# Performance work log

Measured on AMD Instinct MI355X. Metric: run time of the kernel, lower is better.

## Reference

```python
import jax, jax.numpy as jnp
from jax import lax
import numpy as np

B, T, I, H, STEPS = 512, 256, 64, 512, 10


def setup_inputs() -> dict:
    key = jax.random.key(0)
    ks = jax.random.split(key, 11)
    k = 1.0 / np.sqrt(H)  # PyTorch default init bound
    u = lambda kk, shape: jax.random.uniform(kk, shape, jnp.float32, -k, k)
    return dict(
        x=jax.random.normal(ks[0], (B, T, I), jnp.float32),
        W_ih0=u(ks[1], (4 * H, I)), W_hh0=u(ks[2], (4 * H, H)),
        b_ih0=u(ks[3], (4 * H,)), b_hh0=u(ks[4], (4 * H,)),
        W_ih1=u(ks[5], (4 * H, H)), W_hh1=u(ks[6], (4 * H, H)),
        b_ih1=u(ks[7], (4 * H,)), b_hh1=u(ks[8], (4 * H,)),
        W_lin=u(ks[9], (I, H)), b_lin=u(ks[10], (I,)),
        future_steps=STEPS,
    )


def _cell(x_t, h, c, W_ih, W_hh, b):
    # PyTorch LSTM gate order: i, f, g, o
    gates = x_t @ W_ih.T + h @ W_hh.T + b
    i, f, g, o = jnp.split(gates, 4, axis=-1)
    c_new = jax.nn.sigmoid(f) * c + jax.nn.sigmoid(i) * jnp.tanh(g)
    h_new = jax.nn.sigmoid(o) * jnp.tanh(c_new)
    return h_new, c_new


def _layer_scan(xs, W_ih, W_hh, b):
    # xs: [B, T, D] -> outputs [B, T, H], final (h, c)
    Bsz, Hd = xs.shape[0], W_hh.shape[1]
    h0 = jnp.zeros((Bsz, Hd), xs.dtype)

    def step(carry, x_t):
        h, c = _cell(x_t, carry[0], carry[1], W_ih, W_hh, b)
        return (h, c), h

    (h, c), ys = lax.scan(step, (h0, h0), jnp.swapaxes(xs, 0, 1))
    return jnp.swapaxes(ys, 0, 1), (h, c)


def reference(x, W_ih0, W_hh0, b_ih0, b_hh0, W_ih1, W_hh1, b_ih1, b_hh1, W_lin, b_lin, future_steps):
    b0 = b_ih0 + b_hh0
    b1 = b_ih1 + b_hh1
    # encoder pass over the conditioning sequence
    ys0, (h0f, c0f) = _layer_scan(x, W_ih0, W_hh0, b0)
    _, (h1f, c1f) = _layer_scan(ys0, W_ih1, W_hh1, b1)
    inp = x[:, -1, :]

    def dec_step(carry, _):
        cur, h0, c0, h1, c1 = carry
        h0, c0 = _cell(cur, h0, c0, W_ih0, W_hh0, b0)
        h1, c1 = _cell(h0, h1, c1, W_ih1, W_hh1, b1)
        out = h1 @ W_lin.T + b_lin  # [B, I]
        return (out, h0, c0, h1, c1), out

    _, outs = lax.scan(dec_step, (inp, h0f, c0f, h1f, c1f), None, length=future_steps)
    return jnp.swapaxes(outs, 0, 1)  # [B, future_steps, I]
```

## Files before the change

kernel.cpp:

```cpp
#include <hip/hip_runtime.h>
#include <stdint.h>

#define BSZ 512
#define TT  256
#define IIN 64
#define HH  512
#define NSTEPS 10
#define NBLOCKS 512

typedef unsigned short ushort_t;
typedef short bf16x8 __attribute__((ext_vector_type(8)));
typedef float f32x4  __attribute__((ext_vector_type(4)));

static constexpr size_t W0TILE = 256*576;
static constexpr size_t W1TILE = 256*1024;
static constexpr size_t N0W = 8*W0TILE;
static constexpr size_t NTW = N0W + 8*W1TILE;

__device__ __forceinline__ ushort_t f2bf(float f){
  union { float f; uint32_t u; } v; v.f = f;
  uint32_t u = v.u;
  return (ushort_t)((u + 0x7fffu + ((u >> 16) & 1u)) >> 16);
}
__device__ __forceinline__ float bf2f(ushort_t h){
  union { uint32_t u; float f; } v; v.u = ((uint32_t)h) << 16;
  return v.f;
}
__device__ __forceinline__ void split2(float f, ushort_t& h, ushort_t& l){
  h = f2bf(f); l = f2bf(f - bf2f(h));
}
__device__ __forceinline__ float sigf(float x){ return 1.0f/(1.0f+__expf(-x)); }
__device__ __forceinline__ float tanhfast(float x){ return 1.0f - 2.0f/(__expf(2.0f*x)+1.0f); }

__device__ __forceinline__ unsigned long long aload64(const uint32_t* p){
  return __hip_atomic_load((const unsigned long long*)(const void*)p,
                           __ATOMIC_RELAXED, __HIP_MEMORY_SCOPE_AGENT);
}
__device__ __forceinline__ void astore32(uint32_t* p, uint32_t v){
  __hip_atomic_store(p, v, __ATOMIC_RELAXED, __HIP_MEMORY_SCOPE_AGENT);
}

__device__ __forceinline__ int get_xcd(){
  unsigned v;
  asm volatile("s_getreg_b32 %0, hwreg(HW_REG_XCC_ID)" : "=s"(v));
  return (int)(v & 7);
}

struct KP {
  const float* x;
  const ushort_t *Wh, *Wl;
  const float *b0v, *b1v;
  const float *Wlin, *blin;
  uint32_t *h0a, *h0b, *h1a, *h1b;
  float *c0m, *c1m;
  uint32_t *outp;
  float* out;
  uint32_t *bar, *rel, *assign;
};

__device__ __forceinline__ int lds_base(int c, int r){ return (c*16 + r)*64; }

__device__ __forceinline__ void stage_packed(ushort_t* lds, const uint32_t* src,
    int rowbase, int stride, int lognu, int cbase)
{
  const int nunits = 1 << lognu;
  const int ntasks = nunits << 4;
  for (int tsk = threadIdx.x; tsk < ntasks; tsk += 256){
    const int r  = tsk >> lognu;
    const int uk = tsk & (nunits-1);
    const uint32_t* sp = src + (size_t)(rowbase + r)*stride + uk*8;
    unsigned long long qq[4];
    qq[0]=aload64(sp); qq[1]=aload64(sp+2); qq[2]=aload64(sp+4); qq[3]=aload64(sp+6);
    union { ushort_t us[8]; bf16x8 v; } H, L;
    #pragma unroll
    for (int i2=0;i2<4;++i2){
      uint32_t a2 = (uint32_t)qq[i2], b2 = (uint32_t)(qq[i2]>>32);
      H.us[2*i2]   = (ushort_t)a2;  L.us[2*i2]   = (ushort_t)(a2>>16);
      H.us[2*i2+1] = (ushort_t)b2;  L.us[2*i2+1] = (ushort_t)(b2>>16);
    }
    const int c = cbase + (uk >> 2);
    const int u = uk & 3;
    const int sh = (u | ((c&1)<<2)) ^ (r&7);
    const int sl = (u | (((c&1)^1)<<2)) ^ (r&7);
    *(bf16x8*)&lds[lds_base(c,r) + sh*8] = H.v;
    *(bf16x8*)&lds[lds_base(c,r) + sl*8] = L.v;
  }
}

__device__ __forceinline__ void stage_f32(ushort_t* lds, const float* src,
    int rowbase, int stride, int cbase)
{
  const int tsk = threadIdx.x;
  if (tsk < 128){
    const int r = tsk >> 3, uk = tsk & 7;
    const float* sp = src + (size_t)(rowbase + r)*stride + uk*8;
    f32x4 v0 = *(const f32x4*)sp, v1 = *(const f32x4*)(sp+4);
    union { ushort_t us[8]; bf16x8 v; } H, L;
    #pragma unroll
    for (int i2=0;i2<4;++i2){
      split2(v0[i2], H.us[i2],   L.us[i2]);
      split2(v1[i2], H.us[4+i2], L.us[4+i2]);
    }
    const int c = cbase + (uk >> 2);
    const int u = uk & 3;
    const int sh = (u | ((c&1)<<2)) ^ (r&7);
    const int sl = (u | (((c&1)^1)<<2)) ^ (r&7);
    *(bf16x8*)&lds[lds_base(c,r) + sh*8] = H.v;
    *(bf16x8*)&lds[lds_base(c,r) + sl*8] = L.v;
  }
}

__device__ __forceinline__ void cell_compute(const ushort_t* lds,
    const ushort_t* __restrict__ wh, const ushort_t* __restrict__ wl, int nch,
    int m, int n, const float* bias, float* c4, float* cmem, uint32_t* houtp)
{
  const int tid = threadIdx.x;
  const int w = tid >> 6, l = tid & 63;
  const int lr = l & 15, kq = l >> 4;
  f32x4 acc[4];
  #pragma unroll
  for (int s=0;s<4;++s) acc[s] = (f32x4){0.f,0.f,0.f,0.f};

  const int clb = w*64 + lr;
  for (int c = 0; c < nch; ++c){
    const int shi = (kq | ((c&1)<<2)) ^ (lr&7);
    const int slo = (kq | (((c&1)^1)<<2)) ^ (lr&7);
    bf16x8 ah = *(const bf16x8*)&lds[lds_base(c,lr) + shi*8];
    bf16x8 al = *(const bf16x8*)&lds[lds_base(c,lr) + slo*8];
    #pragma unroll
    for (int s=0;s<4;++s){
      size_t bo = ((size_t)(c*256 + clb + s*16))*32 + kq*8;
      bf16x8 bh = *(const bf16x8*)&wh[bo];
      bf16x8 bl = *(const bf16x8*)&wl[bo];
      acc[s] = __builtin_amdgcn_mfma_f32_16x16x32_bf16(ah, bh, acc[s],0,0,0);
      acc[s] = __builtin_amdgcn_mfma_f32_16x16x32_bf16(ah, bl, acc[s],0,0,0);
      acc[s] = __builtin_amdgcn_mfma_f32_16x16x32_bf16(al, bh, acc[s],0,0,0);
    }
  }

  const int j = n*64 + w*16 + lr;
  const float bi = bias[j], bf = bias[512+j], bg = bias[1024+j], bo2 = bias[1536+j];
  #pragma unroll
  for (int q=0;q<4;++q){
    const int row = m*16 + kq*4 + q;
    float gi = acc[0][q]+bi, gf = acc[1][q]+bf, gg = acc[2][q]+bg, go = acc[3][q]+bo2;
    const size_t cidx = ((size_t)row << 9) + j;
    float cold = cmem ? cmem[cidx] : c4[q];
    float cn = sigf(gf)*cold + sigf(gi)*tanhfast(gg);
    if (cmem) cmem[cidx] = cn; else c4[q] = cn;
    float hv = sigf(go)*tanhfast(cn);
    ushort_t hh2, hl2; split2(hv, hh2, hl2);
    astore32(&houtp[cidx], (uint32_t)hh2 | ((uint32_t)hl2 << 16));
  }
}

__device__ __forceinline__ void role0_step(const KP& p, ushort_t* lds, int m, int n,
    const float* xsrc, const uint32_t* osrc,
    const uint32_t* h0r, uint32_t* h0w, float* c4, float* cmem)
{
  if (xsrc) stage_f32(lds, xsrc, m*16, TT*IIN, 0);
  else      stage_packed(lds, osrc, m*16, 64, 3, 0);
  stage_packed(lds, h0r, m*16, 512, 6, 2);
  __syncthreads();
  cell_compute(lds, p.Wh + (size_t)n*W0TILE, p.Wl + (size_t)n*W0TILE, 18,
               m, n, p.b0v, c4, cmem, h0w);
}

__device__ __forceinline__ void role1_step(const KP& p, ushort_t* lds, int m, int n,
    const uint32_t* h0cur, const uint32_t* h1r, uint32_t* h1w, float* c4, float* cmem)
{
  stage_packed(lds, h0cur, m*16, 512, 6, 0);
  stage_packed(lds, h1r,   m*16, 512, 6, 16);
  __syncthreads();
  cell_compute(lds, p.Wh + N0W + (size_t)n*W1TILE, p.Wl + N0W + (size_t)n*W1TILE, 32,
               m, n, p.b1v, c4, cmem, h1w);
}

__device__ __forceinline__ void lin_step(const KP& p, ushort_t* lds, int m, int d,
                                         const uint32_t* h1cur)
{
  float* lf = (float*)lds;
  const int r0 = m*16;
  for (int tsk = threadIdx.x; tsk < 4096; tsk += 256){
    const int r = tsk >> 8, e2 = (tsk & 255)*2;
    unsigned long long q = aload64(h1cur + (size_t)(r0+r)*512 + e2);
    uint32_t a2 = (uint32_t)q, b2 = (uint32_t)(q>>32);
    lf[r*512 + e2]     = bf2f((ushort_t)a2) + bf2f((ushort_t)(a2>>16));
    lf[r*512 + e2 + 1] = bf2f((ushort_t)b2) + bf2f((ushort_t)(b2>>16));
  }
  __syncthreads();
  const int i = threadIdx.x & 63;
  const int rq = threadIdx.x >> 6;
  const float* wr = p.Wlin + (size_t)i*512;
  float sum[4] = {0.f,0.f,0.f,0.f};
  for (int k = 0; k < 512; k += 4){
    f32x4 wv = *(const f32x4*)(wr + k);
    #pragma unroll
    for (int q2=0;q2<4;++q2){
      const float* hfp = &lf[(rq*4+q2)*512 + k];
      sum[q2] += hfp[0]*wv[0] + hfp[1]*wv[1] + hfp[2]*wv[2] + hfp[3]*wv[3];
    }
  }
  #pragma unroll
  for (int q2=0;q2<4;++q2){
    const int row = r0 + rq*4 + q2;
    float v = sum[q2] + p.blin[i];
    p.out[(size_t)row*(NSTEPS*IIN) + d*IIN + i] = v;
    ushort_t oh, ol; split2(v, oh, ol);
    astore32(&p.outp[row*64 + i], (uint32_t)oh | ((uint32_t)ol<<16));
  }
  __syncthreads();
}

__global__ __launch_bounds__(256, 2)
void lstm_persist(KP p)
{
  __shared__ ushort_t lds[32768];
  __shared__ int s_lt;
  if (threadIdx.x == 0){
    const int xcd = get_xcd();
    int lt = 0;
    for (int a = 0; a < 8; ++a){
      const int xx = (xcd + a) & 7;
      uint32_t idx = __hip_atomic_fetch_add(&p.assign[xx], 1u, __ATOMIC_RELAXED,
                                            __HIP_MEMORY_SCOPE_AGENT);
      if (idx < 64u){ lt = xx*64 + (int)idx; break; }
    }
    s_lt = lt;
  }
  __syncthreads();
  const int lt = s_lt;
  const int n = lt >> 6;
  const int li = lt & 63;
  const int role = li >> 5;
  const int m = li & 31;

  float c4[4] = {0.f,0.f,0.f,0.f};
  uint32_t* h0[2] = { p.h0a, p.h0b };
  uint32_t* h1[2] = { p.h1a, p.h1b };

  int slot = 0;
  auto gbar = [&](){
    __syncthreads();
    if (threadIdx.x == 0){
      uint32_t old = __hip_atomic_fetch_add(&p.bar[slot], 1u, __ATOMIC_RELAXED,
                                            __HIP_MEMORY_SCOPE_AGENT);
      if (old == (uint32_t)(NBLOCKS-1)){
        __hip_atomic_store(&p.rel[slot], 1u, __ATOMIC_RELAXED, __HIP_MEMORY_SCOPE_AGENT);
      } else {
        while (!__hip_atomic_load(&p.rel[slot], __ATOMIC_RELAXED, __HIP_MEMORY_SCOPE_AGENT))
          __builtin_amdgcn_s_sleep(1);
      }
    }
    __syncthreads();
    ++slot;
  };

  for (int s = 0; s <= TT; ++s){
    if (role == 0 && s < TT){
      role0_step(p, lds, m, n, p.x + (size_t)s*IIN, nullptr,
                 h0[(s+1)&1], h0[s&1], c4, nullptr);
    } else if (role == 1 && s >= 1){
      const int t = s-1;
      role1_step(p, lds, m, n, h0[t&1], h1[(t+1)&1], h1[t&1], c4, nullptr);
    }
    gbar();
  }
  int p0 = 1, p1 = 1;
  for (int d = 0; d < NSTEPS; ++d){
    if (role == 0){
      if (d == 0) role0_step(p, lds, m, n, p.x + (size_t)(TT-1)*IIN, nullptr,
                             h0[p0], h0[1-p0], c4, nullptr);
      else        role0_step(p, lds, m, n, nullptr, p.outp,
                             h0[p0], h0[1-p0], c4, nullptr);
    }
    gbar();
    if (role == 1) role1_step(p, lds, m, n, h0[1-p0], h1[p1], h1[1-p1], c4, nullptr);
    gbar();
    if (role == 0 && n == 0) lin_step(p, lds, m, d, h1[1-p1]);
    gbar();
    p0 ^= 1; p1 ^= 1;
  }
}

__global__ __launch_bounds__(256, 2)
void fb_enc(KP p, int s){
  __shared__ ushort_t lds[32768];
  uint32_t* h0[2] = { p.h0a, p.h0b };
  uint32_t* h1[2] = { p.h1a, p.h1b };
  const int bid = blockIdx.x;
  const int role = bid >> 8, tile = bid & 255, m = tile >> 3, n = tile & 7;
  if (role == 0 && s < TT)
    role0_step(p, lds, m, n, p.x + (size_t)s*IIN, nullptr,
               h0[(s+1)&1], h0[s&1], nullptr, p.c0m);
  else if (role == 1 && s >= 1){
    const int t = s-1;
    role1_step(p, lds, m, n, h0[t&1], h1[(t+1)&1], h1[t&1], nullptr, p.c1m);
  }
}
__global__ __launch_bounds__(256, 2)
void fb_dec0(KP p, int d, int p0){
  __shared__ ushort_t lds[32768];
  uint32_t* h0[2] = { p.h0a, p.h0b };
  const int m = blockIdx.x >> 3, n = blockIdx.x & 7;
  if (d == 0) role0_step(p, lds, m, n, p.x + (size_t)(TT-1)*IIN, nullptr,
                         h0[p0], h0[1-p0], nullptr, p.c0m);
  else        role0_step(p, lds, m, n, nullptr, p.outp,
                         h0[p0], h0[1-p0], nullptr, p.c0m);
}
__global__ __launch_bounds__(256, 2)
void fb_dec1(KP p, int p0, int p1){
  __shared__ ushort_t lds[32768];
  uint32_t* h0[2] = { p.h0a, p.h0b };
  uint32_t* h1[2] = { p.h1a, p.h1b };
  const int m = blockIdx.x >> 3, n = blockIdx.x & 7;
  role1_step(p, lds, m, n, h0[1-p0], h1[p1], h1[1-p1], nullptr, p.c1m);
}
__global__ __launch_bounds__(256)
void fb_lin(KP p, int d, int p1){
  __shared__ ushort_t lds[32768];
  uint32_t* h1[2] = { p.h1a, p.h1b };
  lin_step(p, lds, blockIdx.x, d, h1[1-p1]);
}

__global__ void bias_kernel(const float* a, const float* b, float* o){
  int i = blockIdx.x * 256 + threadIdx.x;
  if (i < 2048) o[i] = a[i] + b[i];
}

__global__ void prep_w(const float* __restrict__ Wih0, const float* __restrict__ Whh0,
                       const float* __restrict__ Wih1, const float* __restrict__ Whh1,
                       ushort_t* __restrict__ Wh, ushort_t* __restrict__ Wl)
{
  size_t i = (size_t)blockIdx.x*256 + threadIdx.x;
  if (i >= NTW) return;
  float val;
  if (i < N0W){
    int n   = (int)(i / W0TILE);
    int rem = (int)(i % W0TILE);
    int c   = rem / 8192;
    int rem2= rem & 8191;
    int cl  = rem2 >> 5;
    int q   = rem2 & 31;
    int k   = c*32 + q;
    int grow = ((cl>>4)&3)*512 + n*64 + ((cl>>6)&3)*16 + (cl&15);
    val = (k < 64) ? Wih0[(size_t)grow*64 + k] : Whh0[(size_t)grow*512 + (k-64)];
  } else {
    size_t e = i - N0W;
    int n   = (int)(e / W1TILE);
    int rem = (int)(e % W1TILE);
    int c   = rem / 8192;
    int rem2= rem & 8191;
    int cl  = rem2 >> 5;
    int q   = rem2 & 31;
    int k   = c*32 + q;
    int grow = ((cl>>4)&3)*512 + n*64 + ((cl>>6)&3)*16 + (cl&15);
    val = (k < 512) ? Wih1[(size_t)grow*512 + k] : Whh1[(size_t)grow*512 + (k-512)];
  }
  ushort_t h, lo2; split2(val, h, lo2);
  Wh[i] = h; Wl[i] = lo2;
}

extern "C" void kernel_launch(void* const* d_in, const int* in_sizes, int n_in,
                              void* d_out, int out_size, void* d_ws, size_t ws_size,
                              hipStream_t stream)
{
  const float* x     = (const float*)d_in[0];
  const float* W_ih0 = (const float*)d_in[1];
  const float* W_hh0 = (const float*)d_in[2];
  const float* b_ih0 = (const float*)d_in[3];
  const float* b_hh0 = (const float*)d_in[4];
  const float* W_ih1 = (const float*)d_in[5];
  const float* W_hh1 = (const float*)d_in[6];
  const float* b_ih1 = (const float*)d_in[7];
  const float* b_hh1 = (const float*)d_in[8];
  const float* W_lin = (const float*)d_in[9];
  const float* b_lin = (const float*)d_in[10];

  char* ws = (char*)d_ws;
  size_t off = 0;
  auto alloc = [&](size_t bytes){ size_t o = off; off += (bytes + 255) & ~(size_t)255; return o; };

  float* b0v = (float*)(ws + alloc(2048*4));
  float* b1v = (float*)(ws + alloc(2048*4));
  ushort_t* Wh = (ushort_t*)(ws + alloc(NTW*2));
  ushort_t* Wl = (ushort_t*)(ws + alloc(NTW*2));

  const size_t BH = (size_t)BSZ * HH;
  size_t statesBytes = 4*BH*4 + 2*BH*4 + (size_t)BSZ*IIN*4 + 512*4 + 512*4 + 16*4;
  char* states = ws + alloc(statesBytes);
  uint32_t* h0a = (uint32_t*)states;
  uint32_t* h0b = h0a + BH;
  uint32_t* h1a = h0a + 2*BH;
  uint32_t* h1b = h0a + 3*BH;
  float* c0m = (float*)(h0a + 4*BH);
  float* c1m = c0m + BH;
  uint32_t* outp = (uint32_t*)(c0m + 2*BH);
  uint32_t* bar  = outp + (size_t)BSZ*IIN;
  uint32_t* rel  = bar + 512;
  uint32_t* assign = rel + 512;

  bias_kernel<<<8, 256, 0, stream>>>(b_ih0, b_hh0, b0v);
  bias_kernel<<<8, 256, 0, stream>>>(b_ih1, b_hh1, b1v);
  prep_w<<<(int)((NTW+255)/256), 256, 0, stream>>>(W_ih0, W_hh0, W_ih1, W_hh1, Wh, Wl);
  hipMemsetAsync(states, 0, statesBytes, stream);

  KP kp;
  kp.x = x; kp.Wh = Wh; kp.Wl = Wl; kp.b0v = b0v; kp.b1v = b1v;
  kp.Wlin = W_lin; kp.blin = b_lin;
  kp.h0a = h0a; kp.h0b = h0b; kp.h1a = h1a; kp.h1b = h1b;
  kp.c0m = c0m; kp.c1m = c1m; kp.outp = outp;
  kp.out = (float*)d_out;
  kp.bar = bar; kp.rel = rel; kp.assign = assign;

  void* kargs[] = { &kp };
  hipError_t ce = hipLaunchCooperativeKernel((void*)lstm_persist,
                                             dim3(NBLOCKS), dim3(256), kargs, 0, stream);
  if (ce != hipSuccess){
    for (int s = 0; s <= TT; ++s)
      fb_enc<<<NBLOCKS, 256, 0, stream>>>(kp, s);
    int p0 = 1, p1 = 1;
    for (int d = 0; d < NSTEPS; ++d){
      fb_dec0<<<256, 256, 0, stream>>>(kp, d, p0);
      fb_dec1<<<256, 256, 0, stream>>>(kp, p0, p1);
      fb_lin<<<32, 256, 0, stream>>>(kp, d, p1);
      p0 ^= 1; p1 ^= 1;
    }
  }
}
```

Measured before the change: 10.26 ms.

## Merge layer roles into one block per tile and use a hierarchical grid barrier

Each persistent block now computes both layer-0 and layer-1 cells for its (m,n) tile, so the grid shrinks from 512 to 256 blocks. All global loads for the staged inputs are issued before any LDS writes, so load latency overlaps, and the chunk loops are fully unrolled through template parameters. The grid barrier now counts arrivals in 8 per-XCD counters that a single master block sums before releasing the rest, which cuts contention on one atomic. The trade-off is that each block does serial work for both layers per encoder step and has half as many waves to hide latency.

```diff
diff --git a/kernel.cpp b/kernel.cpp
--- a/kernel.cpp
+++ b/kernel.cpp
@@ -6,7 +6,7 @@
 #define IIN 64
 #define HH  512
 #define NSTEPS 10
-#define NBLOCKS 512
+#define NBLOCKS 256
 
 typedef unsigned short ushort_t;
 typedef short bf16x8 __attribute__((ext_vector_type(8)));
@@ -38,6 +38,9 @@
 }
 __device__ __forceinline__ void astore32(uint32_t* p, uint32_t v){
   __hip_atomic_store(p, v, __ATOMIC_RELAXED, __HIP_MEMORY_SCOPE_AGENT);
+}
+__device__ __forceinline__ uint32_t aload32(const uint32_t* p){
+  return __hip_atomic_load(p, __ATOMIC_RELAXED, __HIP_MEMORY_SCOPE_AGENT);
 }
 
 __device__ __forceinline__ int get_xcd(){
@@ -60,123 +63,179 @@
 
 __device__ __forceinline__ int lds_base(int c, int r){ return (c*16 + r)*64; }
 
-__device__ __forceinline__ void stage_packed(ushort_t* lds, const uint32_t* src,
-    int rowbase, int stride, int lognu, int cbase)
-{
-  const int nunits = 1 << lognu;
-  const int ntasks = nunits << 4;
-  for (int tsk = threadIdx.x; tsk < ntasks; tsk += 256){
-    const int r  = tsk >> lognu;
-    const int uk = tsk & (nunits-1);
-    const uint32_t* sp = src + (size_t)(rowbase + r)*stride + uk*8;
-    unsigned long long qq[4];
-    qq[0]=aload64(sp); qq[1]=aload64(sp+2); qq[2]=aload64(sp+4); qq[3]=aload64(sp+6);
-    union { ushort_t us[8]; bf16x8 v; } H, L;
+template<int NU>
+struct StageP {
+  static constexpr int NTASK = NU*16;
+  static constexpr int TPT = (NTASK + 255)/256;
+  unsigned long long q[TPT][4];
+  __device__ __forceinline__ void issue(const uint32_t* src, int rowbase, int stride){
     #pragma unroll
-    for (int i2=0;i2<4;++i2){
-      uint32_t a2 = (uint32_t)qq[i2], b2 = (uint32_t)(qq[i2]>>32);
-      H.us[2*i2]   = (ushort_t)a2;  L.us[2*i2]   = (ushort_t)(a2>>16);
-      H.us[2*i2+1] = (ushort_t)b2;  L.us[2*i2+1] = (ushort_t)(b2>>16);
-    }
-    const int c = cbase + (uk >> 2);
-    const int u = uk & 3;
-    const int sh = (u | ((c&1)<<2)) ^ (r&7);
-    const int sl = (u | (((c&1)^1)<<2)) ^ (r&7);
-    *(bf16x8*)&lds[lds_base(c,r) + sh*8] = H.v;
-    *(bf16x8*)&lds[lds_base(c,r) + sl*8] = L.v;
-  }
-}
-
-__device__ __forceinline__ void stage_f32(ushort_t* lds, const float* src,
-    int rowbase, int stride, int cbase)
-{
-  const int tsk = threadIdx.x;
-  if (tsk < 128){
-    const int r = tsk >> 3, uk = tsk & 7;
-    const float* sp = src + (size_t)(rowbase + r)*stride + uk*8;
-    f32x4 v0 = *(const f32x4*)sp, v1 = *(const f32x4*)(sp+4);
-    union { ushort_t us[8]; bf16x8 v; } H, L;
+    for (int i=0;i<TPT;++i){
+      const int t = i*256 + (int)threadIdx.x;
+      if (NTASK % 256 == 0 || t < NTASK){
+        const int r = t / NU, uk = t - r*NU;
+        const uint32_t* sp = src + (size_t)(rowbase+r)*stride + uk*8;
+        q[i][0]=aload64(sp);   q[i][1]=aload64(sp+2);
+        q[i][2]=aload64(sp+4); q[i][3]=aload64(sp+6);
+      }
+    }
+  }
+  __device__ __forceinline__ void commit(ushort_t* lds, int cbase){
     #pragma unroll
-    for (int i2=0;i2<4;++i2){
-      split2(v0[i2], H.us[i2],   L.us[i2]);
-      split2(v1[i2], H.us[4+i2], L.us[4+i2]);
-    }
-    const int c = cbase + (uk >> 2);
-    const int u = uk & 3;
-    const int sh = (u | ((c&1)<<2)) ^ (r&7);
-    const int sl = (u | (((c&1)^1)<<2)) ^ (r&7);
-    *(bf16x8*)&lds[lds_base(c,r) + sh*8] = H.v;
-    *(bf16x8*)&lds[lds_base(c,r) + sl*8] = L.v;
-  }
-}
-
-__device__ __forceinline__ void cell_compute(const ushort_t* lds,
-    const ushort_t* __restrict__ wh, const ushort_t* __restrict__ wl, int nch,
-    int m, int n, const float* bias, float* c4, float* cmem, uint32_t* houtp)
+    for (int i=0;i<TPT;++i){
+      const int t = i*256 + (int)threadIdx.x;
+      if (NTASK % 256 == 0 || t < NTASK){
+        const int r = t / NU, uk = t - r*NU;
+        union { ushort_t us[8]; bf16x8 v; } H, L;
+        #pragma unroll
+        for (int j=0;j<4;++j){
+          uint32_t a2=(uint32_t)q[i][j], b2=(uint32_t)(q[i][j]>>32);
+          H.us[2*j]  =(ushort_t)a2; L.us[2*j]  =(ushort_t)(a2>>16);
+          H.us[2*j+1]=(ushort_t)b2; L.us[2*j+1]=(ushort_t)(b2>>16);
+        }
+        const int c = cbase + (uk>>2), u = uk&3;
+        const int sh = (u | ((c&1)<<2)) ^ (r&7);
+        const int sl = (u | (((c&1)^1)<<2)) ^ (r&7);
+        *(bf16x8*)&lds[lds_base(c,r)+sh*8] = H.v;
+        *(bf16x8*)&lds[lds_base(c,r)+sl*8] = L.v;
+      }
+    }
+  }
+};
+
+struct StageF {
+  f32x4 v0, v1;
+  __device__ __forceinline__ void issue(const float* src, int rowbase, int stride){
+    const int t = threadIdx.x;
+    if (t < 128){
+      const int r = t>>3, uk = t&7;
+      const float* sp = src + (size_t)(rowbase+r)*stride + uk*8;
+      v0 = *(const f32x4*)sp; v1 = *(const f32x4*)(sp+4);
+    }
+  }
+  __device__ __forceinline__ void commit(ushort_t* lds, int cbase){
+    const int t = threadIdx.x;
+    if (t < 128){
+      const int r = t>>3, uk = t&7;
+      union { ushort_t us[8]; bf16x8 v; } H, L;
+      #pragma unroll
+      for (int j=0;j<4;++j){
+        split2(v0[j], H.us[j],   L.us[j]);
+        split2(v1[j], H.us[4+j], L.us[4+j]);
+      }
+      const int c = cbase + (uk>>2), u = uk&3;
+      const int sh = (u | ((c&1)<<2)) ^ (r&7);
+      const int sl = (u | (((c&1)^1)<<2)) ^ (r&7);
+      *(bf16x8*)&lds[lds_base(c,r)+sh*8] = H.v;
+      *(bf16x8*)&lds[lds_base(c,r)+sl*8] = L.v;
+    }
+  }
+};
+
+template<int NCH, int COFS, bool CMEM>
+__device__ __forceinline__ void cell_compute2(const ushort_t* lds,
+    const ushort_t* __restrict__ wh, const ushort_t* __restrict__ wl,
+    int m, const float* bjs, float* cr, float* cmem,
+    uint32_t* houtp, int jcol)
 {
   const int tid = threadIdx.x;
   const int w = tid >> 6, l = tid & 63;
   const int lr = l & 15, kq = l >> 4;
+  const int clb = w*64 + lr;
   f32x4 acc[4];
   #pragma unroll
   for (int s=0;s<4;++s) acc[s] = (f32x4){0.f,0.f,0.f,0.f};
 
-  const int clb = w*64 + lr;
-  for (int c = 0; c < nch; ++c){
-    const int shi = (kq | ((c&1)<<2)) ^ (lr&7);
-    const int slo = (kq | (((c&1)^1)<<2)) ^ (lr&7);
-    bf16x8 ah = *(const bf16x8*)&lds[lds_base(c,lr) + shi*8];
-    bf16x8 al = *(const bf16x8*)&lds[lds_base(c,lr) + slo*8];
+  #pragma unroll
+  for (int c=0;c<NCH;++c){
+    const int cp = c + COFS;
+    const int shi = (kq | ((cp&1)<<2)) ^ (lr&7);
+    const int slo = (kq | (((cp&1)^1)<<2)) ^ (lr&7);
+    const bf16x8 ah = *(const bf16x8*)&lds[lds_base(cp,lr)+shi*8];
+    const bf16x8 al = *(const bf16x8*)&lds[lds_base(cp,lr)+slo*8];
     #pragma unroll
     for (int s=0;s<4;++s){
-      size_t bo = ((size_t)(c*256 + clb + s*16))*32 + kq*8;
-      bf16x8 bh = *(const bf16x8*)&wh[bo];
-      bf16x8 bl = *(const bf16x8*)&wl[bo];
+      const size_t bo = ((size_t)(c*256 + clb + s*16))*32 + kq*8;
+      const bf16x8 bh = *(const bf16x8*)&wh[bo];
+      const bf16x8 bl = *(const bf16x8*)&wl[bo];
       acc[s] = __builtin_amdgcn_mfma_f32_16x16x32_bf16(ah, bh, acc[s],0,0,0);
       acc[s] = __builtin_amdgcn_mfma_f32_16x16x32_bf16(ah, bl, acc[s],0,0,0);
       acc[s] = __builtin_amdgcn_mfma_f32_16x16x32_bf16(al, bh, acc[s],0,0,0);
     }
   }
-
-  const int j = n*64 + w*16 + lr;
-  const float bi = bias[j], bf = bias[512+j], bg = bias[1024+j], bo2 = bias[1536+j];
   #pragma unroll
   for (int q=0;q<4;++q){
     const int row = m*16 + kq*4 + q;
-    float gi = acc[0][q]+bi, gf = acc[1][q]+bf, gg = acc[2][q]+bg, go = acc[3][q]+bo2;
-    const size_t cidx = ((size_t)row << 9) + j;
-    float cold = cmem ? cmem[cidx] : c4[q];
+    float gi = acc[0][q]+bjs[0], gf = acc[1][q]+bjs[1];
+    float gg = acc[2][q]+bjs[2], go = acc[3][q]+bjs[3];
+    const size_t cidx = ((size_t)row << 9) + jcol;
+    float cold = CMEM ? cmem[cidx] : cr[q];
     float cn = sigf(gf)*cold + sigf(gi)*tanhfast(gg);
-    if (cmem) cmem[cidx] = cn; else c4[q] = cn;
+    if (CMEM) cmem[cidx] = cn; else cr[q] = cn;
     float hv = sigf(go)*tanhfast(cn);
     ushort_t hh2, hl2; split2(hv, hh2, hl2);
     astore32(&houtp[cidx], (uint32_t)hh2 | ((uint32_t)hl2 << 16));
   }
 }
 
-__device__ __forceinline__ void role0_step(const KP& p, ushort_t* lds, int m, int n,
-    const float* xsrc, const uint32_t* osrc,
-    const uint32_t* h0r, uint32_t* h0w, float* c4, float* cmem)
-{
-  if (xsrc) stage_f32(lds, xsrc, m*16, TT*IIN, 0);
-  else      stage_packed(lds, osrc, m*16, 64, 3, 0);
-  stage_packed(lds, h0r, m*16, 512, 6, 2);
-  __syncthreads();
-  cell_compute(lds, p.Wh + (size_t)n*W0TILE, p.Wl + (size_t)n*W0TILE, 18,
-               m, n, p.b0v, c4, cmem, h0w);
-}
-
-__device__ __forceinline__ void role1_step(const KP& p, ushort_t* lds, int m, int n,
-    const uint32_t* h0cur, const uint32_t* h1r, uint32_t* h1w, float* c4, float* cmem)
-{
-  stage_packed(lds, h0cur, m*16, 512, 6, 0);
-  stage_packed(lds, h1r,   m*16, 512, 6, 16);
-  __syncthreads();
-  cell_compute(lds, p.Wh + N0W + (size_t)n*W1TILE, p.Wl + N0W + (size_t)n*W1TILE, 32,
-               m, n, p.b1v, c4, cmem, h1w);
-}
-
-__device__ __forceinline__ void lin_step(const KP& p, ushort_t* lds, int m, int d,
+template<bool CMEM>
+__device__ __forceinline__ void enc_body(const KP& p, ushort_t* lds, int m, int n, int s,
+    const float* b0r, const float* b1r, float* c0r, float* c1r, int jcol)
+{
+  uint32_t* h0[2] = { p.h0a, p.h0b };
+  uint32_t* h1[2] = { p.h1a, p.h1b };
+  const uint32_t* rd0 = h0[(s+1)&1];
+  uint32_t* wr0 = h0[s&1];
+  const uint32_t* rd1 = h1[s&1];
+  uint32_t* wr1 = h1[(s+1)&1];
+  StageF SX; StageP<64> S0; StageP<64> S1;
+  if (s < TT) SX.issue(p.x + (size_t)s*IIN, m*16, TT*IIN);
+  S0.issue(rd0, m*16, 512);
+  if (s >= 1) S1.issue(rd1, m*16, 512);
+  if (s < TT) SX.commit(lds, 0);
+  S0.commit(lds, 2);
+  if (s >= 1) S1.commit(lds, 18);
+  __syncthreads();
+  if (s < TT)
+    cell_compute2<18,0,CMEM>(lds, p.Wh + (size_t)n*W0TILE, p.Wl + (size_t)n*W0TILE,
+                             m, b0r, c0r, p.c0m, wr0, jcol);
+  if (s >= 1)
+    cell_compute2<32,2,CMEM>(lds, p.Wh + N0W + (size_t)n*W1TILE, p.Wl + N0W + (size_t)n*W1TILE,
+                             m, b1r, c1r, p.c1m, wr1, jcol);
+}
+
+template<bool CMEM>
+__device__ __forceinline__ void dec0_body(const KP& p, ushort_t* lds, int m, int n, int d, int p0,
+    const float* b0r, float* c0r, int jcol)
+{
+  uint32_t* h0[2] = { p.h0a, p.h0b };
+  StageF SX; StageP<8> SO; StageP<64> S0;
+  if (d == 0) SX.issue(p.x + (size_t)(TT-1)*IIN, m*16, TT*IIN);
+  else        SO.issue(p.outp, m*16, 64);
+  S0.issue(h0[p0], m*16, 512);
+  if (d == 0) SX.commit(lds, 0); else SO.commit(lds, 0);
+  S0.commit(lds, 2);
+  __syncthreads();
+  cell_compute2<18,0,CMEM>(lds, p.Wh + (size_t)n*W0TILE, p.Wl + (size_t)n*W0TILE,
+                           m, b0r, c0r, p.c0m, h0[1-p0], jcol);
+}
+
+template<bool CMEM>
+__device__ __forceinline__ void dec1_body(const KP& p, ushort_t* lds, int m, int n, int p0, int p1,
+    const float* b1r, float* c1r, int jcol)
+{
+  uint32_t* h0[2] = { p.h0a, p.h0b };
+  uint32_t* h1[2] = { p.h1a, p.h1b };
+  StageP<64> SA; StageP<64> SB;
+  SA.issue(h0[1-p0], m*16, 512);
+  SB.issue(h1[p1], m*16, 512);
+  SA.commit(lds, 2); SB.commit(lds, 18);
+  __syncthreads();
+  cell_compute2<32,2,CMEM>(lds, p.Wh + N0W + (size_t)n*W1TILE, p.Wl + N0W + (size_t)n*W1TILE,
+                           m, b1r, c1r, p.c1m, h1[1-p1], jcol);
+}
+
+__device__ __forceinline__ void lin_body(const KP& p, ushort_t* lds, int m, int d,
                                          const uint32_t* h1cur)
 {
   float* lf = (float*)lds;
@@ -215,7 +274,7 @@
 __global__ __launch_bounds__(256, 2)
 void lstm_persist(KP p)
 {
-  __shared__ ushort_t lds[32768];
+  __shared__ ushort_t lds[34816];
   __shared__ int s_lt;
   if (threadIdx.x == 0){
     const int xcd = get_xcd();
@@ -224,32 +283,40 @@
       const int xx = (xcd + a) & 7;
       uint32_t idx = __hip_atomic_fetch_add(&p.assign[xx], 1u, __ATOMIC_RELAXED,
                                             __HIP_MEMORY_SCOPE_AGENT);
-      if (idx < 64u){ lt = xx*64 + (int)idx; break; }
+      if (idx < 32u){ lt = xx*32 + (int)idx; break; }
     }
     s_lt = lt;
   }
   __syncthreads();
   const int lt = s_lt;
-  const int n = lt >> 6;
-  const int li = lt & 63;
-  const int role = li >> 5;
-  const int m = li & 31;
-
-  float c4[4] = {0.f,0.f,0.f,0.f};
-  uint32_t* h0[2] = { p.h0a, p.h0b };
-  uint32_t* h1[2] = { p.h1a, p.h1b };
-
+  const int n = lt >> 5;
+  const int m = lt & 31;
+
+  const int jcol = n*64 + ((threadIdx.x >> 6) * 16) + (threadIdx.x & 15);
+  float b0r[4] = { p.b0v[jcol], p.b0v[512+jcol], p.b0v[1024+jcol], p.b0v[1536+jcol] };
+  float b1r[4] = { p.b1v[jcol], p.b1v[512+jcol], p.b1v[1024+jcol], p.b1v[1536+jcol] };
+  float c0r[4] = {0.f,0.f,0.f,0.f};
+  float c1r[4] = {0.f,0.f,0.f,0.f};
+
+  const int bid = blockIdx.x;
+  const int lane8 = bid & 7;
   int slot = 0;
   auto gbar = [&](){
     __syncthreads();
     if (threadIdx.x == 0){
-      uint32_t old = __hip_atomic_fetch_add(&p.bar[slot], 1u, __ATOMIC_RELAXED,
-                                            __HIP_MEMORY_SCOPE_AGENT);
-      if (old == (uint32_t)(NBLOCKS-1)){
+      __hip_atomic_fetch_add(&p.bar[slot*8 + lane8], 1u, __ATOMIC_RELAXED,
+                             __HIP_MEMORY_SCOPE_AGENT);
+      if (bid == 0){
+        for (;;){
+          uint32_t s2 = 0;
+          #pragma unroll
+          for (int j2=0;j2<8;++j2) s2 += aload32(&p.bar[slot*8 + j2]);
+          if (s2 == (uint32_t)NBLOCKS) break;
+          __builtin_amdgcn_s_sleep(1);
+        }
         __hip_atomic_store(&p.rel[slot], 1u, __ATOMIC_RELAXED, __HIP_MEMORY_SCOPE_AGENT);
       } else {
-        while (!__hip_atomic_load(&p.rel[slot], __ATOMIC_RELAXED, __HIP_MEMORY_SCOPE_AGENT))
-          __builtin_amdgcn_s_sleep(1);
+        while (!aload32(&p.rel[slot])) __builtin_amdgcn_s_sleep(1);
       }
     }
     __syncthreads();
@@ -257,27 +324,17 @@
   };
 
   for (int s = 0; s <= TT; ++s){
-    if (role == 0 && s < TT){
-      role0_step(p, lds, m, n, p.x + (size_t)s*IIN, nullptr,
-                 h0[(s+1)&1], h0[s&1], c4, nullptr);
-    } else if (role == 1 && s >= 1){
-      const int t = s-1;
-      role1_step(p, lds, m, n, h0[t&1], h1[(t+1)&1], h1[t&1], c4, nullptr);
-    }
+    enc_body<false>(p, lds, m, n, s, b0r, b1r, c0r, c1r, jcol);
     gbar();
   }
   int p0 = 1, p1 = 1;
+  uint32_t* h1[2] = { p.h1a, p.h1b };
   for (int d = 0; d < NSTEPS; ++d){
-    if (role == 0){
-      if (d == 0) role0_step(p, lds, m, n, p.x + (size_t)(TT-1)*IIN, nullptr,
-                             h0[p0], h0[1-p0], c4, nullptr);
-      else        role0_step(p, lds, m, n, nullptr, p.outp,
-                             h0[p0], h0[1-p0], c4, nullptr);
-    }
+    dec0_body<false>(p, lds, m, n, d, p0, b0r, c0r, jcol);
     gbar();
-    if (role == 1) role1_step(p, lds, m, n, h0[1-p0], h1[p1], h1[1-p1], c4, nullptr);
+    dec1_body<false>(p, lds, m, n, p0, p1, b1r, c1r, jcol);
     gbar();
-    if (role == 0 && n == 0) lin_step(p, lds, m, d, h1[1-p1]);
+    if (n == 0) lin_body(p, lds, m, d, h1[1-p1]);
     gbar();
     p0 ^= 1; p1 ^= 1;
   }
@@ -285,42 +342,34 @@
 
 __global__ __launch_bounds__(256, 2)
 void fb_enc(KP p, int s){
-  __shared__ ushort_t lds[32768];
-  uint32_t* h0[2] = { p.h0a, p.h0b };
-  uint32_t* h1[2] = { p.h1a, p.h1b };
-  const int bid = blockIdx.x;
-  const int role = bid >> 8, tile = bid & 255, m = tile >> 3, n = tile & 7;
-  if (role == 0 && s < TT)
-    role0_step(p, lds, m, n, p.x + (size_t)s*IIN, nullptr,
-               h0[(s+1)&1], h0[s&1], nullptr, p.c0m);
-  else if (role == 1 && s >= 1){
-    const int t = s-1;
-    role1_step(p, lds, m, n, h0[t&1], h1[(t+1)&1], h1[t&1], nullptr, p.c1m);
-  }
+  __shared__ ushort_t lds[34816];
+  const int m = blockIdx.x >> 3, n = blockIdx.x & 7;
+  const int jcol = n*64 + ((threadIdx.x >> 6) * 16) + (threadIdx.x & 15);
+  float b0r[4] = { p.b0v[jcol], p.b0v[512+jcol], p.b0v[1024+jcol], p.b0v[1536+jcol] };
+  float b1r[4] = { p.b1v[jcol], p.b1v[512+jcol], p.b1v[1024+jcol], p.b1v[1536+jcol] };
+  enc_body<true>(p, lds, m, n, s, b0r, b1r, nullptr, nullptr, jcol);
 }
 __global__ __launch_bounds__(256, 2)
 void fb_dec0(KP p, int d, int p0){
-  __shared__ ushort_t lds[32768];
-  uint32_t* h0[2] = { p.h0a, p.h0b };
+  __shared__ ushort_t lds[34816];
   const int m = blockIdx.x >> 3, n = blockIdx.x & 7;
-  if (d == 0) role0_step(p, lds, m, n, p.x + (size_t)(TT-1)*IIN, nullptr,
-                         h0[p0], h0[1-p0], nullptr, p.c0m);
-  else        role0_step(p, lds, m, n, nullptr, p.outp,
-                         h0[p0], h0[1-p0], nullptr, p.c0m);
+  const int jcol = n*64 + ((threadIdx.x >> 6) * 16) + (threadIdx.x & 15);
+  float b0r[4] = { p.b0v[jcol], p.b0v[512+jcol], p.b0v[1024+jcol], p.b0v[1536+jcol] };
+  dec0_body<true>(p, lds, m, n, d, p0, b0r, nullptr, jcol);
 }
 __global__ __launch_bounds__(256, 2)
 void fb_dec1(KP p, int p0, int p1){
-  __shared__ ushort_t lds[32768];
-  uint32_t* h0[2] = { p.h0a, p.h0b };
-  uint32_t* h1[2] = { p.h1a, p.h1b };
+  __shared__ ushort_t lds[34816];
   const int m = blockIdx.x >> 3, n = blockIdx.x & 7;
-  role1_step(p, lds, m, n, h0[1-p0], h1[p1], h1[1-p1], nullptr, p.c1m);
+  const int jcol = n*64 + ((threadIdx.x >> 6) * 16) + (threadIdx.x & 15);
+  float b1r[4] = { p.b1v[jcol], p.b1v[512+jcol], p.b1v[1024+jcol], p.b1v[1536+jcol] };
+  dec1_body<true>(p, lds, m, n, p0, p1, b1r, nullptr, jcol);
 }
 __global__ __launch_bounds__(256)
 void fb_lin(KP p, int d, int p1){
-  __shared__ ushort_t lds[32768];
+  __shared__ ushort_t lds[34816];
   uint32_t* h1[2] = { p.h1a, p.h1b };
-  lin_step(p, lds, blockIdx.x, d, h1[1-p1]);
+  lin_body(p, lds, blockIdx.x, d, h1[1-p1]);
 }
 
 __global__ void bias_kernel(const float* a, const float* b, float* o){
@@ -387,7 +436,7 @@
   ushort_t* Wl = (ushort_t*)(ws + alloc(NTW*2));
 
   const size_t BH = (size_t)BSZ * HH;
-  size_t statesBytes = 4*BH*4 + 2*BH*4 + (size_t)BSZ*IIN*4 + 512*4 + 512*4 + 16*4;
+  size_t statesBytes = 4*BH*4 + 2*BH*4 + (size_t)BSZ*IIN*4 + 4096*4 + 512*4 + 16*4;
   char* states = ws + alloc(statesBytes);
   uint32_t* h0a = (uint32_t*)states;
   uint32_t* h0b = h0a + BH;
@@ -397,7 +446,7 @@
   float* c1m = c0m + BH;
   uint32_t* outp = (uint32_t*)(c0m + 2*BH);
   uint32_t* bar  = outp + (size_t)BSZ*IIN;
-  uint32_t* rel  = bar + 512;
+  uint32_t* rel  = bar + 4096;
   uint32_t* assign = rel + 512;
 
   bias_kernel<<<8, 256, 0, stream>>>(b_ih0, b_hh0, b0v);
@@ -421,8 +470,8 @@
       fb_enc<<<NBLOCKS, 256, 0, stream>>>(kp, s);
     int p0 = 1, p1 = 1;
     for (int d = 0; d < NSTEPS; ++d){
-      fb_dec0<<<256, 256, 0, stream>>>(kp, d, p0);
-      fb_dec1<<<256, 256, 0, stream>>>(kp, p0, p1);
+      fb_dec0<<<NBLOCKS, 256, 0, stream>>>(kp, d, p0);
+      fb_dec1<<<NBLOCKS, 256, 0, stream>>>(kp, p0, p1);
       fb_lin<<<32, 256, 0, stream>>>(kp, d, p1);
       p0 ^= 1; p1 ^= 1;
     }
```

After: 34.11 ms. +232.3%, slower.

## Replace global grid barrier with per-row-group barriers and batch staging loads

Applied to the files above, without the earlier changes.

The grid-wide barrier, where all 512 blocks hit one counter and then spin on a release flag, is replaced by a monotonic counter per batch-row group. Only the 16 blocks that share rows m (8 column tiles × 2 layer roles) sync with each other, which cuts atomic contention and stops unrelated groups from stalling one another. Staging of h and x into LDS is split into an issue phase that starts all global loads and a commit phase that writes LDS, so loads overlap better. The cost is more registers held per thread, and correctness now relies on row groups being independent and on the group counters starting at zero each launch.

```diff
diff --git a/kernel.cpp b/kernel.cpp
--- a/kernel.cpp
+++ b/kernel.cpp
@@ -38,6 +38,9 @@
 }
 __device__ __forceinline__ void astore32(uint32_t* p, uint32_t v){
   __hip_atomic_store(p, v, __ATOMIC_RELAXED, __HIP_MEMORY_SCOPE_AGENT);
+}
+__device__ __forceinline__ uint32_t aload32(const uint32_t* p){
+  return __hip_atomic_load(p, __ATOMIC_RELAXED, __HIP_MEMORY_SCOPE_AGENT);
 }
 
 __device__ __forceinline__ int get_xcd(){
@@ -60,55 +63,74 @@
 
 __device__ __forceinline__ int lds_base(int c, int r){ return (c*16 + r)*64; }
 
-__device__ __forceinline__ void stage_packed(ushort_t* lds, const uint32_t* src,
-    int rowbase, int stride, int lognu, int cbase)
-{
-  const int nunits = 1 << lognu;
-  const int ntasks = nunits << 4;
-  for (int tsk = threadIdx.x; tsk < ntasks; tsk += 256){
-    const int r  = tsk >> lognu;
-    const int uk = tsk & (nunits-1);
-    const uint32_t* sp = src + (size_t)(rowbase + r)*stride + uk*8;
-    unsigned long long qq[4];
-    qq[0]=aload64(sp); qq[1]=aload64(sp+2); qq[2]=aload64(sp+4); qq[3]=aload64(sp+6);
-    union { ushort_t us[8]; bf16x8 v; } H, L;
+template<int NU>
+struct StageP {
+  static constexpr int NTASK = NU*16;
+  static constexpr int TPT = (NTASK + 255)/256;
+  unsigned long long q[TPT][4];
+  __device__ __forceinline__ void issue(const uint32_t* src, int rowbase, int stride){
     #pragma unroll
-    for (int i2=0;i2<4;++i2){
-      uint32_t a2 = (uint32_t)qq[i2], b2 = (uint32_t)(qq[i2]>>32);
-      H.us[2*i2]   = (ushort_t)a2;  L.us[2*i2]   = (ushort_t)(a2>>16);
-      H.us[2*i2+1] = (ushort_t)b2;  L.us[2*i2+1] = (ushort_t)(b2>>16);
-    }
-    const int c = cbase + (uk >> 2);
-    const int u = uk & 3;
-    const int sh = (u | ((c&1)<<2)) ^ (r&7);
-    const int sl = (u | (((c&1)^1)<<2)) ^ (r&7);
-    *(bf16x8*)&lds[lds_base(c,r) + sh*8] = H.v;
-    *(bf16x8*)&lds[lds_base(c,r) + sl*8] = L.v;
-  }
-}
-
-__device__ __forceinline__ void stage_f32(ushort_t* lds, const float* src,
-    int rowbase, int stride, int cbase)
-{
-  const int tsk = threadIdx.x;
-  if (tsk < 128){
-    const int r = tsk >> 3, uk = tsk & 7;
-    const float* sp = src + (size_t)(rowbase + r)*stride + uk*8;
-    f32x4 v0 = *(const f32x4*)sp, v1 = *(const f32x4*)(sp+4);
-    union { ushort_t us[8]; bf16x8 v; } H, L;
+    for (int i=0;i<TPT;++i){
+      const int t = i*256 + (int)threadIdx.x;
+      if (NTASK % 256 == 0 || t < NTASK){
+        const int r = t / NU, uk = t - r*NU;
+        const uint32_t* sp = src + (size_t)(rowbase+r)*stride + uk*8;
+        q[i][0]=aload64(sp);   q[i][1]=aload64(sp+2);
+        q[i][2]=aload64(sp+4); q[i][3]=aload64(sp+6);
+      }
+    }
+  }
+  __device__ __forceinline__ void commit(ushort_t* lds, int cbase){
     #pragma unroll
-    for (int i2=0;i2<4;++i2){
-      split2(v0[i2], H.us[i2],   L.us[i2]);
-      split2(v1[i2], H.us[4+i2], L.us[4+i2]);
-    }
-    const int c = cbase + (uk >> 2);
-    const int u = uk & 3;
-    const int sh = (u | ((c&1)<<2)) ^ (r&7);
-    const int sl = (u | (((c&1)^1)<<2)) ^ (r&7);
-    *(bf16x8*)&lds[lds_base(c,r) + sh*8] = H.v;
-    *(bf16x8*)&lds[lds_base(c,r) + sl*8] = L.v;
-  }
-}
+    for (int i=0;i<TPT;++i){
+      const int t = i*256 + (int)threadIdx.x;
+      if (NTASK % 256 == 0 || t < NTASK){
+        const int r = t / NU, uk = t - r*NU;
+        union { ushort_t us[8]; bf16x8 v; } H, L;
+        #pragma unroll
+        for (int j=0;j<4;++j){
+          uint32_t a2=(uint32_t)q[i][j], b2=(uint32_t)(q[i][j]>>32);
+          H.us[2*j]  =(ushort_t)a2; L.us[2*j]  =(ushort_t)(a2>>16);
+          H.us[2*j+1]=(ushort_t)b2; L.us[2*j+1]=(ushort_t)(b2>>16);
+        }
+        const int c = cbase + (uk>>2), u = uk&3;
+        const int sh = (u | ((c&1)<<2)) ^ (r&7);
+        const int sl = (u | (((c&1)^1)<<2)) ^ (r&7);
+        *(bf16x8*)&lds[lds_base(c,r)+sh*8] = H.v;
+        *(bf16x8*)&lds[lds_base(c,r)+sl*8] = L.v;
+      }
+    }
+  }
+};
+
+struct StageF {
+  f32x4 v0, v1;
+  __device__ __forceinline__ void issue(const float* src, int rowbase, int stride){
+    const int t = threadIdx.x;
+    if (t < 128){
+      const int r = t>>3, uk = t&7;
+      const float* sp = src + (size_t)(rowbase+r)*stride + uk*8;
+      v0 = *(const f32x4*)sp; v1 = *(const f32x4*)(sp+4);
+    }
+  }
+  __device__ __forceinline__ void commit(ushort_t* lds, int cbase){
+    const int t = threadIdx.x;
+    if (t < 128){
+      const int r = t>>3, uk = t&7;
+      union { ushort_t us[8]; bf16x8 v; } H, L;
+      #pragma unroll
+      for (int j=0;j<4;++j){
+        split2(v0[j], H.us[j],   L.us[j]);
+        split2(v1[j], H.us[4+j], L.us[4+j]);
+      }
+      const int c = cbase + (uk>>2), u = uk&3;
+      const int sh = (u | ((c&1)<<2)) ^ (r&7);
+      const int sl = (u | (((c&1)^1)<<2)) ^ (r&7);
+      *(bf16x8*)&lds[lds_base(c,r)+sh*8] = H.v;
+      *(bf16x8*)&lds[lds_base(c,r)+sl*8] = L.v;
+    }
+  }
+};
 
 __device__ __forceinline__ void cell_compute(const ushort_t* lds,
     const ushort_t* __restrict__ wh, const ushort_t* __restrict__ wl, int nch,
@@ -158,9 +180,12 @@
     const float* xsrc, const uint32_t* osrc,
     const uint32_t* h0r, uint32_t* h0w, float* c4, float* cmem)
 {
-  if (xsrc) stage_f32(lds, xsrc, m*16, TT*IIN, 0);
-  else      stage_packed(lds, osrc, m*16, 64, 3, 0);
-  stage_packed(lds, h0r, m*16, 512, 6, 2);
+  StageF SX; StageP<8> SO; StageP<64> S0;
+  if (xsrc) SX.issue(xsrc, m*16, TT*IIN);
+  else      SO.issue(osrc, m*16, 64);
+  S0.issue(h0r, m*16, 512);
+  if (xsrc) SX.commit(lds, 0); else SO.commit(lds, 0);
+  S0.commit(lds, 2);
   __syncthreads();
   cell_compute(lds, p.Wh + (size_t)n*W0TILE, p.Wl + (size_t)n*W0TILE, 18,
                m, n, p.b0v, c4, cmem, h0w);
@@ -169,8 +194,11 @@
 __device__ __forceinline__ void role1_step(const KP& p, ushort_t* lds, int m, int n,
     const uint32_t* h0cur, const uint32_t* h1r, uint32_t* h1w, float* c4, float* cmem)
 {
-  stage_packed(lds, h0cur, m*16, 512, 6, 0);
-  stage_packed(lds, h1r,   m*16, 512, 6, 16);
+  StageP<64> SA; StageP<64> SB;
+  SA.issue(h0cur, m*16, 512);
+  SB.issue(h1r,   m*16, 512);
+  SA.commit(lds, 0);
+  SB.commit(lds, 16);
   __syncthreads();
   cell_compute(lds, p.Wh + N0W + (size_t)n*W1TILE, p.Wl + N0W + (size_t)n*W1TILE, 32,
                m, n, p.b1v, c4, cmem, h1w);
@@ -239,21 +267,16 @@
   uint32_t* h0[2] = { p.h0a, p.h0b };
   uint32_t* h1[2] = { p.h1a, p.h1b };
 
-  int slot = 0;
+  uint32_t* grpline = &p.bar[m*16];
+  uint32_t target = 0;
   auto gbar = [&](){
     __syncthreads();
     if (threadIdx.x == 0){
-      uint32_t old = __hip_atomic_fetch_add(&p.bar[slot], 1u, __ATOMIC_RELAXED,
-                                            __HIP_MEMORY_SCOPE_AGENT);
-      if (old == (uint32_t)(NBLOCKS-1)){
-        __hip_atomic_store(&p.rel[slot], 1u, __ATOMIC_RELAXED, __HIP_MEMORY_SCOPE_AGENT);
-      } else {
-        while (!__hip_atomic_load(&p.rel[slot], __ATOMIC_RELAXED, __HIP_MEMORY_SCOPE_AGENT))
-          __builtin_amdgcn_s_sleep(1);
-      }
+      target += 16;
+      __hip_atomic_fetch_add(grpline, 1u, __ATOMIC_RELAXED, __HIP_MEMORY_SCOPE_AGENT);
+      while (aload32(grpline) < target) __builtin_amdgcn_s_sleep(1);
     }
     __syncthreads();
-    ++slot;
   };
 
   for (int s = 0; s <= TT; ++s){
```

New measurement: 9.941 ms. 3.2% less time.
